# Performance work log

Hardware: AMD Instinct MI355X
Metric: run time of the kernel (lower is better)

Reference implementation:

```python
import jax, jax.numpy as jnp
import numpy as np

D_MODEL = 1024
NUM_HEADS = 16
HEAD_DIM = D_MODEL // NUM_HEADS
B, S, S_CACHE = 2, 2048, 2048


def setup_inputs() -> dict:
    key = jax.random.key(0)
    ks = jax.random.split(key, 7)
    scale = 1.0 / np.sqrt(D_MODEL)
    return {
        "x": jax.random.normal(ks[0], (B, S, D_MODEL), dtype=jnp.float32),
        "kv_k": jax.random.normal(ks[1], (B, NUM_HEADS, S_CACHE, HEAD_DIM), dtype=jnp.float32),
        "kv_v": jax.random.normal(ks[2], (B, NUM_HEADS, S_CACHE, HEAD_DIM), dtype=jnp.float32),
        "W_Q": jax.random.normal(ks[3], (D_MODEL, D_MODEL), dtype=jnp.float32) * scale,
        "W_K": jax.random.normal(ks[4], (D_MODEL, D_MODEL), dtype=jnp.float32) * scale,
        "W_V": jax.random.normal(ks[5], (D_MODEL, D_MODEL), dtype=jnp.float32) * scale,
        "W_O": jax.random.normal(ks[6], (D_MODEL, D_MODEL), dtype=jnp.float32) * scale,
    }


def reference(x, kv_k, kv_v, W_Q, W_K, W_V, W_O):
    b, s, d = x.shape
    h, hd = NUM_HEADS, HEAD_DIM
    # projections: [B,S,D] -> [B,H,S,hd]
    def proj(W):
        return jnp.einsum('bsd,de->bse', x, W).reshape(b, s, h, hd).transpose(0, 2, 1, 3)
    Q = proj(W_Q)
    K = proj(W_K)
    V = proj(W_V)
    # KV-cache concat along sequence axis
    K = jnp.concatenate([kv_k, K], axis=2)  # [B,H,S_tot,hd]
    V = jnp.concatenate([kv_v, V], axis=2)
    scores = jnp.einsum('bhqd,bhkd->bhqk', Q, K) / jnp.sqrt(jnp.float32(hd))
    attn = jax.nn.softmax(scores, axis=-1)
    out = jnp.einsum('bhqk,bhkd->bhqd', attn, V)  # [B,H,S,hd]
    out = out.transpose(0, 2, 1, 3).reshape(b, s, d)
    out = jnp.einsum('bsd,de->bse', out, W_O)
    return (out, (K, V))
```

## Files before the change

kernel.cpp:

```cpp
#include <hip/hip_runtime.h>
#include <hip/hip_bf16.h>

typedef unsigned int u32;
typedef unsigned short u16;
typedef __bf16 bf16x8 __attribute__((ext_vector_type(8)));
typedef float f32x4 __attribute__((ext_vector_type(4)));

typedef const __attribute__((address_space(1))) u32 gas_u32;
typedef __attribute__((address_space(3))) u32 las_u32;

#define ST 4096

__device__ __forceinline__ u16 f2bf(float f) {
    u32 u = __builtin_bit_cast(u32, f);
    u32 r = (u + 0x7FFFu + ((u >> 16) & 1u)) >> 16;
    return (u16)r;
}

__device__ __forceinline__ u32 cvtpk(float lo, float hi) {
    u32 r;
    asm("v_cvt_pk_bf16_f32 %0, %1, %2" : "=v"(r) : "v"(lo), "v"(hi));
    return r;
}

__device__ __forceinline__ uint4 pack8(float4 a, float4 b) {
    uint4 o;
    u16* e = (u16*)&o;
    e[0] = f2bf(a.x); e[1] = f2bf(a.y); e[2] = f2bf(a.z); e[3] = f2bf(a.w);
    e[4] = f2bf(b.x); e[5] = f2bf(b.y); e[6] = f2bf(b.z); e[7] = f2bf(b.w);
    return o;
}

__device__ __forceinline__ void gload_lds16(const u16* g, u16* l) {
    __builtin_amdgcn_global_load_lds((gas_u32*)g, (las_u32*)l, 16, 0, 0);
}

__global__ __launch_bounds__(256) void k_cvt_x(const float* __restrict__ x, u16* __restrict__ xb) {
    int t = blockIdx.x * 256 + threadIdx.x;
    const float4* s = (const float4*)(x + t * 8);
    *(uint4*)(xb + t * 8) = pack8(s[0], s[1]);
}

__global__ __launch_bounds__(256) void k_transpose(const float* w0, const float* w1,
                                                   const float* w2, const float* w3, u16* wt) {
    int z = blockIdx.z;
    const float* W = (z == 0) ? w0 : (z == 1) ? w1 : (z == 2) ? w2 : w3;
    u16* WT = wt + z * (1024 * 1024);
    __shared__ u16 tile[64 * 72];
    int t = threadIdx.x;
    int tr = blockIdx.y * 64, tc = blockIdx.x * 64;
#pragma unroll
    for (int p = 0; p < 2; ++p) {
        int r = (t >> 3) + p * 32, c8 = (t & 7) * 8;
        const float4* src = (const float4*)&W[(tr + r) * 1024 + tc + c8];
        *(uint4*)&tile[r * 72 + c8] = pack8(src[0], src[1]);
    }
    __syncthreads();
#pragma unroll
    for (int p = 0; p < 2; ++p) {
        int r = (t >> 3) + p * 32, c8 = (t & 7) * 8;
        uint4 vv;
        u16* e = (u16*)&vv;
#pragma unroll
        for (int j = 0; j < 8; ++j) e[j] = tile[(c8 + j) * 72 + r];
        *(uint4*)&WT[(tc + r) * 1024 + tr + c8] = vv;
    }
}

__global__ __launch_bounds__(256) void k_copy_cache_t(const float* __restrict__ k_in,
                                                      const float* __restrict__ v_in,
                                                      float* kc, float* vc,
                                                      u16* kb, u16* vbT) {
    __shared__ u16 tile[64 * 72];
    const int t = threadIdx.x;
    const int kt = blockIdx.x, bh = blockIdx.y;
    const int r = t >> 3, c8 = (t & 7) * 8;
#pragma unroll
    for (int p = 0; p < 2; ++p) {
        int rr = r + p * 32;
        int srow = (bh * 2048 + kt * 64 + rr) * 64 + c8;
        int drow = (bh * 4096 + kt * 64 + rr) * 64 + c8;
        const float4* ks = (const float4*)&k_in[srow];
        const float4* vs = (const float4*)&v_in[srow];
        float4 k0 = ks[0], k1 = ks[1], v0 = vs[0], v1 = vs[1];
        *(float4*)&kc[drow] = k0; *(float4*)&kc[drow + 4] = k1;
        *(float4*)&vc[drow] = v0; *(float4*)&vc[drow + 4] = v1;
        *(uint4*)&kb[drow] = pack8(k0, k1);
        *(uint4*)&tile[rr * 72 + c8] = pack8(v0, v1);
    }
    __syncthreads();
#pragma unroll
    for (int p = 0; p < 2; ++p) {
        int dd = r + p * 32;
        uint4 vv;
        u16* e = (u16*)&vv;
#pragma unroll
        for (int j = 0; j < 8; ++j) e[j] = tile[(c8 + j) * 72 + dd];
        *(uint4*)&vbT[(bh * 64 + dd) * 4096 + kt * 64 + c8] = vv;
    }
}

__global__ __launch_bounds__(256) void k_vt(const u16* __restrict__ vbn, u16* __restrict__ vbT) {
    __shared__ u16 tile[64 * 72];
    const int t = threadIdx.x;
    const int kt = blockIdx.x, bh = blockIdx.y;
    const int r = t >> 3, c8 = (t & 7) * 8;
#pragma unroll
    for (int p = 0; p < 2; ++p) {
        int rr = r + p * 32;
        *(uint4*)&tile[rr * 72 + c8] =
            *(const uint4*)&vbn[(bh * 2048 + kt * 64 + rr) * 64 + c8];
    }
    __syncthreads();
#pragma unroll
    for (int p = 0; p < 2; ++p) {
        int dd = r + p * 32;
        uint4 vv;
        u16* e = (u16*)&vv;
#pragma unroll
        for (int j = 0; j < 8; ++j) e[j] = tile[(c8 + j) * 72 + dd];
        *(uint4*)&vbT[(bh * 64 + dd) * 4096 + 2048 + kt * 64 + c8] = vv;
    }
}

__device__ __forceinline__ void gemm_loop(const u16* A, const u16* BT, int mrow, int ncol,
                                          u16* lds_a, u16* lds_b, f32x4 (&acc)[4][4]) {
    const int t = threadIdx.x;
    const int lane = t & 63;
    const int w = t >> 6;
    const int wm = (w >> 1) * 64, wn = (w & 1) * 64;
    const int l15 = lane & 15, lg = lane >> 4;

    const u16* gA = A + (mrow + (t >> 2)) * 1024 + (t & 3) * 8;
    const u16* gB = BT + (ncol + (t >> 2)) * 1024 + (t & 3) * 8;
    u16* la = lds_a + t * 8;
    u16* lb = lds_b + t * 8;

    for (int k0 = 0; k0 < 1024; k0 += 32) {
        gload_lds16(gA + k0, la);
        gload_lds16(gA + k0 + 64 * 1024, la + 64 * 32);
        gload_lds16(gB + k0, lb);
        gload_lds16(gB + k0 + 64 * 1024, lb + 64 * 32);
        __syncthreads();
        bf16x8 af[4], bfr[4];
#pragma unroll
        for (int m = 0; m < 4; ++m)
            af[m] = *(const bf16x8*)&lds_a[(wm + m * 16 + l15) * 32 + lg * 8];
#pragma unroll
        for (int n = 0; n < 4; ++n)
            bfr[n] = *(const bf16x8*)&lds_b[(wn + n * 16 + l15) * 32 + lg * 8];
#pragma unroll
        for (int m = 0; m < 4; ++m)
#pragma unroll
            for (int n = 0; n < 4; ++n)
                acc[m][n] = __builtin_amdgcn_mfma_f32_16x16x32_bf16(af[m], bfr[n], acc[m][n], 0, 0, 0);
        __syncthreads();
    }
}

__global__ __launch_bounds__(256) void k_gemm_qkv(const u16* X, const u16* WT,
                                                  u16* qb, float* kc, float* vc,
                                                  u16* kb, u16* vbn) {
    __shared__ u16 lds_a[128 * 32];
    __shared__ u16 lds_b[128 * 32];
    const int z = blockIdx.z;
    const int mrow = blockIdx.x * 128, ncol = blockIdx.y * 128;

    f32x4 acc[4][4];
#pragma unroll
    for (int m = 0; m < 4; ++m)
#pragma unroll
        for (int n = 0; n < 4; ++n) acc[m][n] = (f32x4){0.f, 0.f, 0.f, 0.f};

    gemm_loop(X, WT + z * (1024 * 1024), mrow, ncol, lds_a, lds_b, acc);

    const int t = threadIdx.x, lane = t & 63, w = t >> 6;
    const int wm = (w >> 1) * 64, wn = (w & 1) * 64;
    const int l15 = lane & 15, lg = lane >> 4;
#pragma unroll
    for (int m = 0; m < 4; ++m)
#pragma unroll
        for (int n = 0; n < 4; ++n)
#pragma unroll
            for (int r = 0; r < 4; ++r) {
                int gr = mrow + wm + m * 16 + lg * 4 + r;
                int gc = ncol + wn + n * 16 + l15;
                int b = gr >> 11, s = gr & 2047, h = gc >> 6, d = gc & 63;
                if (z == 0) {
                    qb[((b * 16 + h) * 2048 + s) * 64 + d] = f2bf(acc[m][n][r]);
                } else {
                    int idx = ((b * 16 + h) * 4096 + 2048 + s) * 64 + d;
                    if (z == 1) { kc[idx] = acc[m][n][r]; if (kb) kb[idx] = f2bf(acc[m][n][r]); }
                    else {
                        vc[idx] = acc[m][n][r];
                        if (vbn) vbn[((b * 16 + h) * 2048 + s) * 64 + d] = f2bf(acc[m][n][r]);
                    }
                }
            }
}

__global__ __launch_bounds__(256) void k_gemm_o(const u16* A, const u16* WT, float* out) {
    __shared__ u16 lds_a[128 * 32];
    __shared__ u16 lds_b[128 * 32];
    const int mrow = blockIdx.x * 128, ncol = blockIdx.y * 128;

    f32x4 acc[4][4];
#pragma unroll
    for (int m = 0; m < 4; ++m)
#pragma unroll
        for (int n = 0; n < 4; ++n) acc[m][n] = (f32x4){0.f, 0.f, 0.f, 0.f};

    gemm_loop(A, WT, mrow, ncol, lds_a, lds_b, acc);

    const int t = threadIdx.x, lane = t & 63, w = t >> 6;
    const int wm = (w >> 1) * 64, wn = (w & 1) * 64;
    const int l15 = lane & 15, lg = lane >> 4;
#pragma unroll
    for (int m = 0; m < 4; ++m)
#pragma unroll
        for (int n = 0; n < 4; ++n)
#pragma unroll
            for (int r = 0; r < 4; ++r) {
                int gr = mrow + wm + m * 16 + lg * 4 + r;
                int gc = ncol + wn + n * 16 + l15;
                out[gr * 1024 + gc] = acc[m][n][r];
            }
}

#define LOG2E_SCALE 0.18033688f
#define RESCALE_THR 11.0f
__global__ __launch_bounds__(512) void k_attn_c(const u16* __restrict__ qb,
                                                const u16* __restrict__ kb,
                                                const u16* __restrict__ vbT,
                                                u16* __restrict__ aws) {
    __shared__ u16 lk[2][4096];
    __shared__ u16 lv[2][4096];
    __shared__ u16 lp[8][16 * 72];

    const int t = threadIdx.x, lane = t & 63, w = t >> 6;
    const int l15 = lane & 15, lg = lane >> 4;
    const int n = blockIdx.x;
    const int wg = (n & 7) * 64 + (n >> 3);
    const int qt = wg & 15, bh = wg >> 4;
    const int b = bh >> 4, h = bh & 15;

    const u16* Qb  = qb + (bh * 2048 + qt * 128 + w * 16) * 64;
    const u16* Kbh = kb + bh * (ST * 64);
    const u16* VbT = vbT + bh * (64 * ST);

    const int kr = t >> 3, kc8 = t & 7;
    const int swz8 = (kc8 ^ (kr & 7)) * 8;
    const int srcK = kr * 64 + swz8;
    const int srcV = kr * ST + swz8;

    bf16x8 qf[2];
#pragma unroll
    for (int ds = 0; ds < 2; ++ds)
        qf[ds] = *(const bf16x8*)&Qb[l15 * 64 + ds * 32 + lg * 8];

    f32x4 o[4];
    float m_ = -INFINITY, ls = 0.f;
#pragma unroll
    for (int i = 0; i < 4; ++i) o[i] = (f32x4){0.f, 0.f, 0.f, 0.f};

    gload_lds16(Kbh + srcK, &lk[0][t * 8]);
    gload_lds16(VbT + srcV, &lv[0][t * 8]);
    __syncthreads();

    for (int kt = 0; kt < ST / 64; ++kt) {
        const int cur = kt & 1, nxt = cur ^ 1;
        const bool more = (kt + 1 < ST / 64);
        if (more) {
            gload_lds16(Kbh + (kt + 1) * 4096 + srcK, &lk[nxt][t * 8]);
            gload_lds16(VbT + (kt + 1) * 64 + srcV, &lv[nxt][t * 8]);
        }

        f32x4 s[4];
        __builtin_amdgcn_s_setprio(1);
#pragma unroll
        for (int ni = 0; ni < 4; ++ni) {
            f32x4 a = (f32x4){0.f, 0.f, 0.f, 0.f};
#pragma unroll
            for (int ds = 0; ds < 2; ++ds) {
                bf16x8 kf = *(const bf16x8*)&lk[cur][(ni * 16 + l15) * 64 + (((ds * 4 + lg) ^ (l15 & 7)) * 8)];
                a = __builtin_amdgcn_mfma_f32_16x16x32_bf16(kf, qf[ds], a, 0, 0, 0);
            }
            s[ni] = a * LOG2E_SCALE;
        }
        __builtin_amdgcn_s_setprio(0);

        float t0 = fmaxf(fmaxf(s[0][0], s[0][1]), fmaxf(s[0][2], s[0][3]));
        float t1 = fmaxf(fmaxf(s[1][0], s[1][1]), fmaxf(s[1][2], s[1][3]));
        float t2 = fmaxf(fmaxf(s[2][0], s[2][1]), fmaxf(s[2][2], s[2][3]));
        float t3 = fmaxf(fmaxf(s[3][0], s[3][1]), fmaxf(s[3][2], s[3][3]));
        float tm = fmaxf(fmaxf(t0, t1), fmaxf(t2, t3));
        if (__any(tm > m_ + RESCALE_THR)) {
            tm = fmaxf(tm, __shfl_xor(tm, 16));
            tm = fmaxf(tm, __shfl_xor(tm, 32));
            float mn = fmaxf(m_, tm);
            float corr = exp2f(m_ - mn);
            ls *= corr;
            m_ = mn;
#pragma unroll
            for (int r = 0; r < 4; ++r) {
                float cr = __shfl(corr, lg * 4 + r);
#pragma unroll
                for (int dt = 0; dt < 4; ++dt) o[dt][r] *= cr;
            }
        }

#pragma unroll
        for (int ni = 0; ni < 4; ++ni) {
            float p0 = exp2f(s[ni][0] - m_);
            float p1 = exp2f(s[ni][1] - m_);
            float p2 = exp2f(s[ni][2] - m_);
            float p3 = exp2f(s[ni][3] - m_);
            ls += (p0 + p1) + (p2 + p3);
            *(uint2*)&lp[w][l15 * 72 + ni * 16 + lg * 4] = make_uint2(cvtpk(p0, p1), cvtpk(p2, p3));
        }

        bf16x8 pf[2];
#pragma unroll
        for (int kss = 0; kss < 2; ++kss)
            pf[kss] = *(const bf16x8*)&lp[w][l15 * 72 + kss * 32 + lg * 8];
        __builtin_amdgcn_s_setprio(1);
#pragma unroll
        for (int dt = 0; dt < 4; ++dt) {
            const int dd = dt * 16 + l15;
#pragma unroll
            for (int kss = 0; kss < 2; ++kss) {
                bf16x8 vf = *(const bf16x8*)&lv[cur][dd * 64 + (((kss * 4 + lg) ^ (dd & 7)) * 8)];
                o[dt] = __builtin_amdgcn_mfma_f32_16x16x32_bf16(pf[kss], vf, o[dt], 0, 0, 0);
            }
        }
        __builtin_amdgcn_s_setprio(0);

        __syncthreads();
    }

    ls += __shfl_xor(ls, 16);
    ls += __shfl_xor(ls, 32);
    const int qrow = qt * 128 + w * 16 + lg * 4;
#pragma unroll
    for (int r = 0; r < 4; ++r) {
        float lr = __shfl(ls, lg * 4 + r);
        float inv = 1.f / lr;
#pragma unroll
        for (int dt = 0; dt < 4; ++dt) {
            int sg = qrow + r;
            int col = h * 64 + dt * 16 + l15;
            aws[(b * 2048 + sg) * 1024 + col] = f2bf(o[dt][r] * inv);
        }
    }
}

__global__ __launch_bounds__(256) void k_attn(const u16* qb, const float* kc,
                                              const float* vc, u16* aws) {
    __shared__ u16 lk[64 * 72];
    __shared__ u16 lvt[64 * 72];
    __shared__ u16 lp[4][16 * 72];

    const int t = threadIdx.x, lane = t & 63, w = t >> 6;
    const int l15 = lane & 15, lg = lane >> 4;
    const int qt = blockIdx.x;
    const int bh = blockIdx.y;
    const int b = bh >> 4, h = bh & 15;

    const u16* Qb = qb + (bh * 2048 + qt * 64 + w * 16) * 64;
    const float* Kb = kc + bh * (ST * 64);
    const float* Vb = vc + bh * (ST * 64);

    bf16x8 qf[2];
#pragma unroll
    for (int ds = 0; ds < 2; ++ds)
        qf[ds] = *(const bf16x8*)&Qb[l15 * 64 + ds * 32 + lg * 8];

    f32x4 o[4];
    float m_[4], ls[4];
#pragma unroll
    for (int i = 0; i < 4; ++i) { o[i] = (f32x4){0.f, 0.f, 0.f, 0.f}; m_[i] = -INFINITY; ls[i] = 0.f; }

    for (int kt = 0; kt < ST / 64; ++kt) {
        const float* ks = Kb + kt * 64 * 64;
        const float* vs = Vb + kt * 64 * 64;
#pragma unroll
        for (int p = 0; p < 2; ++p) {
            int r = (t >> 3) + p * 32, c8 = (t & 7) * 8;
            const float4* k4 = (const float4*)&ks[r * 64 + c8];
            *(uint4*)&lk[r * 72 + c8] = pack8(k4[0], k4[1]);
            const float4* v4 = (const float4*)&vs[r * 64 + c8];
            uint4 vv = pack8(v4[0], v4[1]);
            const u16* e = (const u16*)&vv;
#pragma unroll
            for (int j = 0; j < 8; ++j) lvt[(c8 + j) * 72 + r] = e[j];
        }
        __syncthreads();

        f32x4 s[4];
#pragma unroll
        for (int ni = 0; ni < 4; ++ni) {
            f32x4 a = (f32x4){0.f, 0.f, 0.f, 0.f};
#pragma unroll
            for (int ds = 0; ds < 2; ++ds) {
                bf16x8 kf = *(const bf16x8*)&lk[(ni * 16 + l15) * 72 + ds * 32 + lg * 8];
                a = __builtin_amdgcn_mfma_f32_16x16x32_bf16(qf[ds], kf, a, 0, 0, 0);
            }
            s[ni] = a * 0.125f;
        }

#pragma unroll
        for (int r = 0; r < 4; ++r) {
            float tm = fmaxf(fmaxf(s[0][r], s[1][r]), fmaxf(s[2][r], s[3][r]));
#pragma unroll
            for (int off = 1; off < 16; off <<= 1) tm = fmaxf(tm, __shfl_xor(tm, off));
            float mn = fmaxf(m_[r], tm);
            float corr = __expf(m_[r] - mn);
            float rs = 0.f;
#pragma unroll
            for (int ni = 0; ni < 4; ++ni) {
                float p = __expf(s[ni][r] - mn);
                s[ni][r] = p;
                rs += p;
            }
#pragma unroll
            for (int off = 1; off < 16; off <<= 1) rs += __shfl_xor(rs, off);
            ls[r] = ls[r] * corr + rs;
            m_[r] = mn;
#pragma unroll
            for (int dt = 0; dt < 4; ++dt) o[dt][r] *= corr;
        }

#pragma unroll
        for (int ni = 0; ni < 4; ++ni)
#pragma unroll
            for (int r = 0; r < 4; ++r)
                lp[w][(lg * 4 + r) * 72 + ni * 16 + l15] = f2bf(s[ni][r]);

#pragma unroll
        for (int dt = 0; dt < 4; ++dt) {
#pragma unroll
            for (int kss = 0; kss < 2; ++kss) {
                bf16x8 pf = *(const bf16x8*)&lp[w][l15 * 72 + kss * 32 + lg * 8];
                bf16x8 vf = *(const bf16x8*)&lvt[(dt * 16 + l15) * 72 + kss * 32 + lg * 8];
                o[dt] = __builtin_amdgcn_mfma_f32_16x16x32_bf16(pf, vf, o[dt], 0, 0, 0);
            }
        }
        __syncthreads();
    }

    const int qrow = qt * 64 + w * 16 + lg * 4;
#pragma unroll
    for (int r = 0; r < 4; ++r) {
        float inv = 1.f / ls[r];
#pragma unroll
        for (int dt = 0; dt < 4; ++dt) {
            int sg = qrow + r;
            int col = h * 64 + dt * 16 + l15;
            aws[(b * 2048 + sg) * 1024 + col] = f2bf(o[dt][r] * inv);
        }
    }
}

__global__ __launch_bounds__(256) void k_copy_cache(const float4* __restrict__ k_in,
                                                    const float4* __restrict__ v_in,
                                                    float4* k_out, float4* v_out) {
    int t = blockIdx.x * 256 + threadIdx.x;
    int bh = t >> 15;
    int i = t & 32767;
    k_out[bh * 65536 + i] = k_in[t];
    v_out[bh * 65536 + i] = v_in[t];
}

extern "C" void kernel_launch(void* const* d_in, const int* in_sizes, int n_in,
                              void* d_out, int out_size, void* d_ws, size_t ws_size,
                              hipStream_t stream) {
    const float* x   = (const float*)d_in[0];
    const float* kvk = (const float*)d_in[1];
    const float* kvv = (const float*)d_in[2];
    const float* wq  = (const float*)d_in[3];
    const float* wk  = (const float*)d_in[4];
    const float* wv  = (const float*)d_in[5];
    const float* wo  = (const float*)d_in[6];

    float* out = (float*)d_out;
    float* kc  = out + 4194304;
    float* vc  = kc + 8388608;

    u16* qb = (u16*)d_out;
    u16* xb = (u16*)d_out + 4194304;

    if (ws_size >= (size_t)50331648) {
        u16* wt  = (u16*)d_ws;
        u16* kb  = wt + 4194304;
        u16* vbT = kb + 8388608;
        u16* vbn = vbT + 8388608;
        u16* aws = vbn;

        k_cvt_x<<<dim3(2048), dim3(256), 0, stream>>>(x, xb);
        k_transpose<<<dim3(16, 16, 4), dim3(256), 0, stream>>>(wq, wk, wv, wo, wt);
        k_copy_cache_t<<<dim3(32, 32), dim3(256), 0, stream>>>(kvk, kvv, kc, vc, kb, vbT);
        k_gemm_qkv<<<dim3(32, 8, 3), dim3(256), 0, stream>>>(xb, wt, qb, kc, vc, kb, vbn);
        k_vt<<<dim3(32, 32), dim3(256), 0, stream>>>(vbn, vbT);
        k_attn_c<<<dim3(512), dim3(512), 0, stream>>>(qb, kb, vbT, aws);
        k_gemm_o<<<dim3(32, 8), dim3(256), 0, stream>>>(aws, wt + 3 * 1048576, out);
    } else {
        u16* wt  = (u16*)d_ws;
        u16* xb2 = wt + 4 * 1048576;
        u16* aws = xb2;

        k_cvt_x<<<dim3(2048), dim3(256), 0, stream>>>(x, xb2);
        k_transpose<<<dim3(16, 16, 4), dim3(256), 0, stream>>>(wq, wk, wv, wo, wt);
        k_copy_cache<<<dim3(4096), dim3(256), 0, stream>>>((const float4*)kvk, (const float4*)kvv,
                                                           (float4*)kc, (float4*)vc);
        k_gemm_qkv<<<dim3(32, 8, 3), dim3(256), 0, stream>>>(xb2, wt, qb, kc, vc, nullptr, nullptr);
        k_attn<<<dim3(32, 32), dim3(256), 0, stream>>>(qb, kc, vc, aws);
        k_gemm_o<<<dim3(32, 8), dim3(256), 0, stream>>>(aws, wt + 3 * 1048576, out);
    }
}
```

Before: 243.6 us.

## Switch attention kernel to 32x32x16 MFMA with 32 query rows per wave

Rewrites the cached-KV attention kernel so each wave handles 32 query rows with 32x32x16 bf16 MFMA instead of 16 rows with 16x16x32 MFMA, and halves the block to 256 threads. Each block still covers 128 queries, and each thread now issues two async K/V tile loads per stage. The P tile in LDS is laid out with an XOR swizzle rather than a padded stride. The goal is fewer MFMA and LDS instructions per unit of work and better reuse of each K/V fragment, at the cost of more accumulator registers per thread and fewer waves per block to hide latency.

```diff
diff --git a/kernel.cpp b/kernel.cpp
--- a/kernel.cpp
+++ b/kernel.cpp
@@ -5,6 +5,7 @@
 typedef unsigned short u16;
 typedef __bf16 bf16x8 __attribute__((ext_vector_type(8)));
 typedef float f32x4 __attribute__((ext_vector_type(4)));
+typedef float f32x16 __attribute__((ext_vector_type(16)));
 
 typedef const __attribute__((address_space(1))) u32 gas_u32;
 typedef __attribute__((address_space(3))) u32 las_u32;
@@ -229,128 +230,131 @@
 
 #define LOG2E_SCALE 0.18033688f
 #define RESCALE_THR 11.0f
-__global__ __launch_bounds__(512) void k_attn_c(const u16* __restrict__ qb,
+__global__ __launch_bounds__(256) void k_attn_d(const u16* __restrict__ qb,
                                                 const u16* __restrict__ kb,
                                                 const u16* __restrict__ vbT,
                                                 u16* __restrict__ aws) {
     __shared__ u16 lk[2][4096];
     __shared__ u16 lv[2][4096];
-    __shared__ u16 lp[8][16 * 72];
+    __shared__ u16 lp[4][2048];
 
     const int t = threadIdx.x, lane = t & 63, w = t >> 6;
-    const int l15 = lane & 15, lg = lane >> 4;
+    const int l31 = lane & 31, hi = lane >> 5;
     const int n = blockIdx.x;
     const int wg = (n & 7) * 64 + (n >> 3);
     const int qt = wg & 15, bh = wg >> 4;
     const int b = bh >> 4, h = bh & 15;
 
-    const u16* Qb  = qb + (bh * 2048 + qt * 128 + w * 16) * 64;
+    const u16* Qb  = qb + (bh * 2048 + qt * 128 + w * 32) * 64;
     const u16* Kbh = kb + bh * (ST * 64);
     const u16* VbT = vbT + bh * (64 * ST);
 
     const int kr = t >> 3, kc8 = t & 7;
     const int swz8 = (kc8 ^ (kr & 7)) * 8;
-    const int srcK = kr * 64 + swz8;
-    const int srcV = kr * ST + swz8;
-
-    bf16x8 qf[2];
-#pragma unroll
-    for (int ds = 0; ds < 2; ++ds)
-        qf[ds] = *(const bf16x8*)&Qb[l15 * 64 + ds * 32 + lg * 8];
-
-    f32x4 o[4];
+    const int srcK0 = kr * 64 + swz8, srcK1 = (32 + kr) * 64 + swz8;
+    const int srcV0 = kr * ST + swz8, srcV1 = (32 + kr) * ST + swz8;
+
+    bf16x8 qf[4];
+#pragma unroll
+    for (int sl = 0; sl < 4; ++sl)
+        qf[sl] = *(const bf16x8*)&Qb[l31 * 64 + sl * 16 + hi * 8];
+
+    f32x16 oA = (f32x16)(0.f), oB = (f32x16)(0.f);
     float m_ = -INFINITY, ls = 0.f;
-#pragma unroll
-    for (int i = 0; i < 4; ++i) o[i] = (f32x4){0.f, 0.f, 0.f, 0.f};
-
-    gload_lds16(Kbh + srcK, &lk[0][t * 8]);
-    gload_lds16(VbT + srcV, &lv[0][t * 8]);
+
+    gload_lds16(Kbh + srcK0, &lk[0][t * 8]);
+    gload_lds16(Kbh + srcK1, &lk[0][2048 + t * 8]);
+    gload_lds16(VbT + srcV0, &lv[0][t * 8]);
+    gload_lds16(VbT + srcV1, &lv[0][2048 + t * 8]);
     __syncthreads();
 
     for (int kt = 0; kt < ST / 64; ++kt) {
         const int cur = kt & 1, nxt = cur ^ 1;
         const bool more = (kt + 1 < ST / 64);
         if (more) {
-            gload_lds16(Kbh + (kt + 1) * 4096 + srcK, &lk[nxt][t * 8]);
-            gload_lds16(VbT + (kt + 1) * 64 + srcV, &lv[nxt][t * 8]);
-        }
-
-        f32x4 s[4];
+            const u16* Kt = Kbh + (kt + 1) * 4096;
+            gload_lds16(Kt + srcK0, &lk[nxt][t * 8]);
+            gload_lds16(Kt + srcK1, &lk[nxt][2048 + t * 8]);
+            const u16* Vt = VbT + (kt + 1) * 64;
+            gload_lds16(Vt + srcV0, &lv[nxt][t * 8]);
+            gload_lds16(Vt + srcV1, &lv[nxt][2048 + t * 8]);
+        }
+
+        f32x16 sA = (f32x16)(0.f), sB = (f32x16)(0.f);
         __builtin_amdgcn_s_setprio(1);
 #pragma unroll
-        for (int ni = 0; ni < 4; ++ni) {
-            f32x4 a = (f32x4){0.f, 0.f, 0.f, 0.f};
-#pragma unroll
-            for (int ds = 0; ds < 2; ++ds) {
-                bf16x8 kf = *(const bf16x8*)&lk[cur][(ni * 16 + l15) * 64 + (((ds * 4 + lg) ^ (l15 & 7)) * 8)];
-                a = __builtin_amdgcn_mfma_f32_16x16x32_bf16(kf, qf[ds], a, 0, 0, 0);
-            }
-            s[ni] = a * LOG2E_SCALE;
+        for (int sl = 0; sl < 4; ++sl) {
+            bf16x8 kf = *(const bf16x8*)&lk[cur][l31 * 64 + (((sl * 2 + hi) ^ (l31 & 7)) * 8)];
+            sA = __builtin_amdgcn_mfma_f32_32x32x16_bf16(kf, qf[sl], sA, 0, 0, 0);
+        }
+#pragma unroll
+        for (int sl = 0; sl < 4; ++sl) {
+            bf16x8 kf = *(const bf16x8*)&lk[cur][(32 + l31) * 64 + (((sl * 2 + hi) ^ (l31 & 7)) * 8)];
+            sB = __builtin_amdgcn_mfma_f32_32x32x16_bf16(kf, qf[sl], sB, 0, 0, 0);
         }
         __builtin_amdgcn_s_setprio(0);
-
-        float t0 = fmaxf(fmaxf(s[0][0], s[0][1]), fmaxf(s[0][2], s[0][3]));
-        float t1 = fmaxf(fmaxf(s[1][0], s[1][1]), fmaxf(s[1][2], s[1][3]));
-        float t2 = fmaxf(fmaxf(s[2][0], s[2][1]), fmaxf(s[2][2], s[2][3]));
-        float t3 = fmaxf(fmaxf(s[3][0], s[3][1]), fmaxf(s[3][2], s[3][3]));
-        float tm = fmaxf(fmaxf(t0, t1), fmaxf(t2, t3));
+        sA = sA * LOG2E_SCALE;
+        sB = sB * LOG2E_SCALE;
+
+        float tm = sA[0];
+#pragma unroll
+        for (int i = 1; i < 16; ++i) tm = fmaxf(tm, sA[i]);
+#pragma unroll
+        for (int i = 0; i < 16; ++i) tm = fmaxf(tm, sB[i]);
         if (__any(tm > m_ + RESCALE_THR)) {
-            tm = fmaxf(tm, __shfl_xor(tm, 16));
-            tm = fmaxf(tm, __shfl_xor(tm, 32));
+#pragma unroll
+            for (int off = 1; off < 64; off <<= 1) tm = fmaxf(tm, __shfl_xor(tm, off));
             float mn = fmaxf(m_, tm);
             float corr = exp2f(m_ - mn);
             ls *= corr;
             m_ = mn;
-#pragma unroll
-            for (int r = 0; r < 4; ++r) {
-                float cr = __shfl(corr, lg * 4 + r);
-#pragma unroll
-                for (int dt = 0; dt < 4; ++dt) o[dt][r] *= cr;
-            }
-        }
-
-#pragma unroll
-        for (int ni = 0; ni < 4; ++ni) {
-            float p0 = exp2f(s[ni][0] - m_);
-            float p1 = exp2f(s[ni][1] - m_);
-            float p2 = exp2f(s[ni][2] - m_);
-            float p3 = exp2f(s[ni][3] - m_);
-            ls += (p0 + p1) + (p2 + p3);
-            *(uint2*)&lp[w][l15 * 72 + ni * 16 + lg * 4] = make_uint2(cvtpk(p0, p1), cvtpk(p2, p3));
-        }
-
-        bf16x8 pf[2];
-#pragma unroll
-        for (int kss = 0; kss < 2; ++kss)
-            pf[kss] = *(const bf16x8*)&lp[w][l15 * 72 + kss * 32 + lg * 8];
+            oA = oA * corr;
+            oB = oB * corr;
+        }
+
+#pragma unroll
+        for (int rq = 0; rq < 4; ++rq) {
+            float a0 = exp2f(sA[rq * 4 + 0] - m_), a1 = exp2f(sA[rq * 4 + 1] - m_);
+            float a2 = exp2f(sA[rq * 4 + 2] - m_), a3 = exp2f(sA[rq * 4 + 3] - m_);
+            ls += (a0 + a1) + (a2 + a3);
+            *(uint2*)&lp[w][l31 * 64 + ((rq ^ (l31 & 7)) * 8) + hi * 4] =
+                make_uint2(cvtpk(a0, a1), cvtpk(a2, a3));
+            float b0 = exp2f(sB[rq * 4 + 0] - m_), b1 = exp2f(sB[rq * 4 + 1] - m_);
+            float b2 = exp2f(sB[rq * 4 + 2] - m_), b3 = exp2f(sB[rq * 4 + 3] - m_);
+            ls += (b0 + b1) + (b2 + b3);
+            *(uint2*)&lp[w][l31 * 64 + (((4 + rq) ^ (l31 & 7)) * 8) + hi * 4] =
+                make_uint2(cvtpk(b0, b1), cvtpk(b2, b3));
+        }
+
+        bf16x8 pA[4];
+#pragma unroll
+        for (int ks = 0; ks < 4; ++ks)
+            pA[ks] = *(const bf16x8*)&lp[w][l31 * 64 + (((ks * 2 + hi) ^ (l31 & 7)) * 8)];
         __builtin_amdgcn_s_setprio(1);
 #pragma unroll
-        for (int dt = 0; dt < 4; ++dt) {
-            const int dd = dt * 16 + l15;
-#pragma unroll
-            for (int kss = 0; kss < 2; ++kss) {
-                bf16x8 vf = *(const bf16x8*)&lv[cur][dd * 64 + (((kss * 4 + lg) ^ (dd & 7)) * 8)];
-                o[dt] = __builtin_amdgcn_mfma_f32_16x16x32_bf16(pf[kss], vf, o[dt], 0, 0, 0);
-            }
+        for (int ks = 0; ks < 4; ++ks) {
+            bf16x8 vf = *(const bf16x8*)&lv[cur][l31 * 64 + (((ks * 2 + hi) ^ (l31 & 7)) * 8)];
+            oA = __builtin_amdgcn_mfma_f32_32x32x16_bf16(pA[ks], vf, oA, 0, 0, 0);
+        }
+#pragma unroll
+        for (int ks = 0; ks < 4; ++ks) {
+            bf16x8 vf = *(const bf16x8*)&lv[cur][(32 + l31) * 64 + (((ks * 2 + hi) ^ (l31 & 7)) * 8)];
+            oB = __builtin_amdgcn_mfma_f32_32x32x16_bf16(pA[ks], vf, oB, 0, 0, 0);
         }
         __builtin_amdgcn_s_setprio(0);
 
         __syncthreads();
     }
 
-    ls += __shfl_xor(ls, 16);
     ls += __shfl_xor(ls, 32);
-    const int qrow = qt * 128 + w * 16 + lg * 4;
-#pragma unroll
-    for (int r = 0; r < 4; ++r) {
-        float lr = __shfl(ls, lg * 4 + r);
-        float inv = 1.f / lr;
-#pragma unroll
-        for (int dt = 0; dt < 4; ++dt) {
-            int sg = qrow + r;
-            int col = h * 64 + dt * 16 + l15;
-            aws[(b * 2048 + sg) * 1024 + col] = f2bf(o[dt][r] * inv);
-        }
+    const int qbase = qt * 128 + w * 32;
+#pragma unroll
+    for (int reg = 0; reg < 16; ++reg) {
+        int q = (reg & 3) + 8 * (reg >> 2) + 4 * hi;
+        float inv = 1.f / __shfl(ls, q);
+        int row = (b * 2048 + qbase + q) * 1024 + h * 64;
+        aws[row + l31]      = f2bf(oA[reg] * inv);
+        aws[row + 32 + l31] = f2bf(oB[reg] * inv);
     }
 }
 
@@ -501,7 +505,7 @@
         k_copy_cache_t<<<dim3(32, 32), dim3(256), 0, stream>>>(kvk, kvv, kc, vc, kb, vbT);
         k_gemm_qkv<<<dim3(32, 8, 3), dim3(256), 0, stream>>>(xb, wt, qb, kc, vc, kb, vbn);
         k_vt<<<dim3(32, 32), dim3(256), 0, stream>>>(vbn, vbT);
-        k_attn_c<<<dim3(512), dim3(512), 0, stream>>>(qb, kb, vbT, aws);
+        k_attn_d<<<dim3(512), dim3(256), 0, stream>>>(qb, kb, vbT, aws);
         k_gemm_o<<<dim3(32, 8), dim3(256), 0, stream>>>(aws, wt + 3 * 1048576, out);
     } else {
         u16* wt  = (u16*)d_ws;
```

After: 246.5 us. About the same (+1.2%).
